# Kernel tuning notes

Hardware: AMD Instinct MI355X
Metric: run time of the kernel (lower is better)

Reference implementation:

```python
import jax, jax.numpy as jnp
import numpy as np

NEG = -1e9  # matches deepblast's -1e10-style boundary fill, fp32-safe


def nw_terminal(theta, A):
    # Soft Needleman-Wunsch forward pass with the softmax (logsumexp) operator,
    # vectorized as an anti-diagonal wavefront scan.
    # theta, A: [N, M]. Returns terminal value V[N, M].
    # Recursion (deepblast): V[i,j] = theta[i-1,j-1] +
    #   lse(A[i-1,j-1] + V[i-1,j], V[i-1,j-1], A[i-1,j-1] + V[i,j-1])
    N, M = theta.shape
    ii = jnp.arange(N + 1)  # row index along a diagonal
    prev2 = jnp.full((N + 1,), NEG, theta.dtype).at[0].set(0.0)  # diagonal k=0: V[0,0]=0
    prev1 = jnp.full((N + 1,), NEG, theta.dtype)                  # diagonal k=1: boundary
    neg1 = jnp.full((1,), NEG, theta.dtype)

    def step(carry, k):
        p2, p1 = carry
        jj = k - ii
        valid = (ii >= 1) & (jj >= 1) & (jj <= M)
        ti = jnp.clip(ii - 1, 0, N - 1)
        tj = jnp.clip(jj - 1, 0, M - 1)
        th = theta[ti, tj]
        a = A[ti, tj]
        up = jnp.concatenate([neg1, p1[:-1]])    # V[i-1, j]
        left = p1                                 # V[i, j-1]
        diag = jnp.concatenate([neg1, p2[:-1]])   # V[i-1, j-1]
        v = jax.nn.logsumexp(jnp.stack([a + up, diag, a + left]), axis=0)
        cur = jnp.where(valid, th + v, NEG)
        return (p1, cur), None

    (_, last), _ = jax.lax.scan(step, (prev2, prev1), jnp.arange(2, N + M + 1))
    return last[N]  # V[N, M]


def nw_decode(theta, A):
    # Expected alignment matrix = d V_terminal / d theta, exactly what
    # NWDecoderCUDA.decode computes via its forward/backward DP passes
    # (gradient taken w.r.t. theta only; A is held fixed).
    f = lambda th: jnp.sum(jax.vmap(nw_terminal)(th, A))
    return jax.grad(f)(theta)


def setup_inputs() -> dict:
    key = jax.random.key(0)
    k1, k2, k3, k4 = jax.random.split(key, 4)
    B, N, M, D = 8, 512, 512, 512
    s = 1.0 / np.sqrt(D)  # keep bilinear scores O(1), as trained embeddings would be
    return {
        "zx": jax.random.normal(k1, (B, N, D), jnp.float32) * s,
        "zy": jax.random.normal(k2, (B, M, D), jnp.float32) * s,
        "gx": jax.random.normal(k3, (B, N, D), jnp.float32) * s,
        "gy": jax.random.normal(k4, (B, M, D), jnp.float32) * s,
    }


def reference(zx, zy, gx, gy):
    theta = jax.nn.softplus(jnp.einsum('bid,bjd->bij', zx, zy))  # match scores [B,N,M]
    A = jax.nn.log_sigmoid(jnp.einsum('bid,bjd->bij', gx, gy))   # gap scores   [B,N,M]
    aln = nw_decode(theta, A)                                     # soft alignment [B,N,M]
    return aln, theta, A
```

## Files before the change

kernel.cpp:

```cpp
#include <hip/hip_runtime.h>
#include <cmath>

#define NEG -1e9f
#define LOG2E 1.44269504088896340736f
constexpr int B = 8, N = 512, M = 512, D = 512;
constexpr size_t NM = (size_t)N * M;

constexpr int NCHUNK = 72;

#define EXP2F(x) __builtin_amdgcn_exp2f(x)
#define LOG2F(x) __builtin_amdgcn_logf(x)

typedef float f32x2 __attribute__((ext_vector_type(2)));

#define GLOAD(dst, ptr) \
    asm volatile("global_load_dwordx2 %0, %1, off" : "=v"(dst) : "v"(ptr))

__device__ __forceinline__ float dpp_shr1(float v) {
    return __int_as_float(__builtin_amdgcn_update_dpp(
        __float_as_int(v), __float_as_int(v), 0x138, 0xf, 0xf, false));
}
__device__ __forceinline__ float dpp_shl1(float v) {
    return __int_as_float(__builtin_amdgcn_update_dpp(
        __float_as_int(v), __float_as_int(v), 0x130, 0xf, 0xf, false));
}

__device__ __forceinline__ int diag_off(int kd) {
    return (kd <= 511) ? ((kd * (kd + 1)) >> 1)
                       : ((int)NM - (((1023 - kd) * (1024 - kd)) >> 1));
}

__global__ __launch_bounds__(256)
void gemm_act_kernel(const float* __restrict__ zx, const float* __restrict__ zy,
                     const float* __restrict__ gx, const float* __restrict__ gy,
                     float* __restrict__ out_theta, float* __restrict__ out_A)
{
    const int bz = blockIdx.z;
    const int b = bz >> 1, which = bz & 1;
    const float* X = (which ? gx : zx) + (size_t)b * N * D;
    const float* Y = (which ? gy : zy) + (size_t)b * M * D;
    float* C = (which ? out_A : out_theta) + (size_t)b * NM;

    __shared__ float Xs[16][68];
    __shared__ float Ys[16][68];

    const int tx = threadIdx.x, ty = threadIdx.y;
    const int t = ty * 16 + tx;
    const int lrow = t >> 2;
    const int lk4 = (t & 3) * 4;
    const int row0 = blockIdx.y * 64, col0 = blockIdx.x * 64;

    float acc[4][4] = {};

    for (int k0 = 0; k0 < D; k0 += 16) {
        const float4 xv = *(const float4*)&X[(row0 + lrow) * D + k0 + lk4];
        const float4 yv = *(const float4*)&Y[(col0 + lrow) * D + k0 + lk4];
        Xs[lk4 + 0][lrow] = xv.x; Xs[lk4 + 1][lrow] = xv.y;
        Xs[lk4 + 2][lrow] = xv.z; Xs[lk4 + 3][lrow] = xv.w;
        Ys[lk4 + 0][lrow] = yv.x; Ys[lk4 + 1][lrow] = yv.y;
        Ys[lk4 + 2][lrow] = yv.z; Ys[lk4 + 3][lrow] = yv.w;
        __syncthreads();
#pragma unroll
        for (int kk = 0; kk < 16; kk++) {
            const float4 a = *(const float4*)&Xs[kk][ty * 4];
            const float4 bb = *(const float4*)&Ys[kk][tx * 4];
            acc[0][0] += a.x * bb.x; acc[0][1] += a.x * bb.y; acc[0][2] += a.x * bb.z; acc[0][3] += a.x * bb.w;
            acc[1][0] += a.y * bb.x; acc[1][1] += a.y * bb.y; acc[1][2] += a.y * bb.z; acc[1][3] += a.y * bb.w;
            acc[2][0] += a.z * bb.x; acc[2][1] += a.z * bb.y; acc[2][2] += a.z * bb.z; acc[2][3] += a.z * bb.w;
            acc[3][0] += a.w * bb.x; acc[3][1] += a.w * bb.y; acc[3][2] += a.w * bb.z; acc[3][3] += a.w * bb.w;
        }
        __syncthreads();
    }

#pragma unroll
    for (int r = 0; r < 4; r++) {
        float4 o;
        float* op = &o.x;
#pragma unroll
        for (int c = 0; c < 4; c++) {
            const float x = acc[r][c];
            const float l = log1pf(expf(-fabsf(x)));
            op[c] = which ? (fminf(x, 0.0f) - l)
                          : (fmaxf(x, 0.0f) + l);
        }
        *(float4*)&C[(size_t)(row0 + ty * 4 + r) * M + col0 + tx * 4] = o;
    }
}

__global__ __launch_bounds__(256)
void reorder_in_kernel(const float* __restrict__ theta, const float* __restrict__ A,
                       float2* __restrict__ TAD)
{
    __shared__ float T[64][67];
    __shared__ float Ag[64][67];
    const int b = blockIdx.z;
    const float* ts = theta + (size_t)b * NM;
    const float* as = A + (size_t)b * NM;
    float2* dst = TAD + (size_t)b * NM;
    const int r0 = blockIdx.y * 64, c0 = blockIdx.x * 64;
    const int t = threadIdx.x, lane = t & 63, wv = t >> 6;

#pragma unroll
    for (int e = 0; e < 16; e++) {
        const int r = wv * 16 + e;
        T[r][lane]  = ts[(size_t)(r0 + r) * M + c0 + lane];
        Ag[r][lane] = as[(size_t)(r0 + r) * M + c0 + lane];
    }
    __syncthreads();
    for (int dd = wv; dd < 127; dd += 4) {
        const int kd = r0 + c0 + dd;
        const int rlo = max(0, dd - 63);
        const int L = min(63, dd) - rlo + 1;
        if (lane < L) {
            const int rloc = rlo + lane;
            const int gr = r0 + rloc;
            dst[diag_off(kd) + gr - max(0, kd - 511)] =
                make_float2(T[rloc][dd - rloc] * LOG2E, Ag[rloc][dd - rloc] * LOG2E);
        }
    }
}

__global__ __launch_bounds__(256)
void reorder_out_kernel(const float* __restrict__ ED, float* __restrict__ aln)
{
    __shared__ float T[64][67];
    const int b = blockIdx.z;
    const float* src = ED + (size_t)b * NM;
    float* dst = aln + (size_t)b * NM;
    const int r0 = blockIdx.y * 64, c0 = blockIdx.x * 64;
    const int t = threadIdx.x, lane = t & 63, wv = t >> 6;

    for (int dd = wv; dd < 127; dd += 4) {
        const int kd = r0 + c0 + dd;
        const int rlo = max(0, dd - 63);
        const int L = min(63, dd) - rlo + 1;
        if (lane < L) {
            const int rloc = rlo + lane;
            const int gr = r0 + rloc;
            T[rloc][dd - rloc] = src[diag_off(kd) + gr - max(0, kd - 511)];
        }
    }
    __syncthreads();
#pragma unroll
    for (int e = 0; e < 16; e++) {
        const int r = wv * 16 + e;
        dst[(size_t)(r0 + r) * M + c0 + lane] = T[r][lane];
    }
}

#define VMCNT_TOP_PF                                        \
    if (pf) { asm volatile("s_waitcnt vmcnt(16)"); }        \
    else    { asm volatile("s_waitcnt vmcnt(0)");  }        \
    __builtin_amdgcn_sched_barrier(0);

#define CHUNK_BARRIER                          \
    __builtin_amdgcn_sched_barrier(0);         \
    asm volatile("s_waitcnt lgkmcnt(0)");      \
    __builtin_amdgcn_s_barrier();              \
    __builtin_amdgcn_sched_barrier(0);

#define DECL16(P)  f32x2 P##0, P##1, P##2, P##3, P##4, P##5, P##6, P##7, \
                         P##8, P##9, P##10, P##11, P##12, P##13, P##14, P##15;
#define DECL16F(P) float P##0, P##1, P##2, P##3, P##4, P##5, P##6, P##7, \
                         P##8, P##9, P##10, P##11, P##12, P##13, P##14, P##15;

#define FLOAD1(dst) {                                          \
    asm volatile("global_load_dwordx2 %0, %1, %2"              \
                 : "=v"(dst) : "v"(off8l), "s"(tab));          \
    const int d_ = (kdl <= 510) ? max(kdl + 1, 0)              \
                                : max(1022 - kdl, 0);          \
    off8l += d_ * 8; kdl++;                                    \
}
#define F_ISSUE(P) {                                           \
    FLOAD1(P##0)  FLOAD1(P##1)  FLOAD1(P##2)  FLOAD1(P##3)     \
    FLOAD1(P##4)  FLOAD1(P##5)  FLOAD1(P##6)  FLOAD1(P##7)     \
    FLOAD1(P##8)  FLOAD1(P##9)  FLOAD1(P##10) FLOAD1(P##11)    \
    FLOAD1(P##12) FLOAD1(P##13) FLOAD1(P##14) FLOAD1(P##15)    \
}

#define F_CORE(kd_, TA, sh1v, dgv, O) {                        \
    const float th = (TA).x, a = (TA).y;                       \
    const float x0 = a + sh1v;                                 \
    const float x2 = a + vprev;                                \
    const float mx = fmaxf(fmaxf(x0, dgv), x2);                \
    const float e0 = EXP2F(x0 - mx);                           \
    const float e1 = EXP2F(dgv - mx);                          \
    const float e2 = EXP2F(x2 - mx);                           \
    const float sum = e0 + e1 + e2;                            \
    const float inv = __builtin_amdgcn_rcpf(sum);              \
    (O).x = e0 * inv; (O).y = e2 * inv;                        \
    vprev = th + mx + LOG2F(sum);                              \
}

#define F_STEP_I(s, TA, O, RG) {                               \
    float sh1 = dpp_shr1(vprev);                               \
    if (lane == 0) sh1 = RG;                                   \
    const float dgv = sh1_d;                                   \
    sh1_d = sh1;                                               \
    F_CORE(kb + (s), TA, sh1, dgv, O)                          \
    wv##s = vprev;                                             \
}

#define F_STEP_G(s, TA, O, RG) {                               \
    const int kd = kb + (s);                                   \
    const int jj = kd - tid;                                   \
    float sh1 = dpp_shr1(vprev);                               \
    if (lane == 0) sh1 = RG;                                   \
    const float dgv = (jj == 0) ? ((tid == 0) ? 0.0f : NEG) : sh1_d; \
    sh1_d = sh1;                                               \
    if (jj >= 0 && jj < M) { F_CORE(kd, TA, sh1, dgv, O) }     \
    wv##s = vprev;                                             \
}

#define F_STEPS(SFX, CUR)                                                      \
    F_STEP_##SFX(0,  CUR##0,  o0,  rgP) F_STEP_##SFX(1,  CUR##1,  o1,  g0)     \
    F_STEP_##SFX(2,  CUR##2,  o2,  g1)  F_STEP_##SFX(3,  CUR##3,  o3,  g2)     \
    F_STEP_##SFX(4,  CUR##4,  o4,  g3)  F_STEP_##SFX(5,  CUR##5,  o5,  g4)     \
    F_STEP_##SFX(6,  CUR##6,  o6,  g5)  F_STEP_##SFX(7,  CUR##7,  o7,  g6)     \
    F_STEP_##SFX(8,  CUR##8,  o8,  g7)  F_STEP_##SFX(9,  CUR##9,  o9,  g8)     \
    F_STEP_##SFX(10, CUR##10, o10, g9)  F_STEP_##SFX(11, CUR##11, o11, g10)    \
    F_STEP_##SFX(12, CUR##12, o12, g11) F_STEP_##SFX(13, CUR##13, o13, g12)    \
    F_STEP_##SFX(14, CUR##14, o14, g13) F_STEP_##SFX(15, CUR##15, o15, g14)

#define F_ADV_S { const int d_ = (kds <= 510) ? (kds + 1) : (1022 - kds);    \
                  off8s += d_ * 8; kds++; }
#define FST_I(O) {                                                           \
    asm volatile("global_store_dwordx2 %0, %1, %2"                           \
                 :: "v"(off8s), "v"(O), "s"(pb) : "memory");                 \
    F_ADV_S }
#define FST_G(s, O) {                                                        \
    const int jj = kb + (s) - tid;                                           \
    if (jj >= 0 && jj < M) {                                                 \
        asm volatile("global_store_dwordx2 %0, %1, %2"                       \
                     :: "v"(off8s), "v"(O), "s"(pb) : "memory"); }           \
    F_ADV_S }
#define F_STORES_I {                                                         \
    FST_I(o0)  FST_I(o1)  FST_I(o2)  FST_I(o3)                               \
    FST_I(o4)  FST_I(o5)  FST_I(o6)  FST_I(o7)                               \
    FST_I(o8)  FST_I(o9)  FST_I(o10) FST_I(o11)                              \
    FST_I(o12) FST_I(o13) FST_I(o14) FST_I(o15) }
#define F_STORES_G {                                                         \
    FST_G(0,o0)   FST_G(1,o1)   FST_G(2,o2)   FST_G(3,o3)                    \
    FST_G(4,o4)   FST_G(5,o5)   FST_G(6,o6)   FST_G(7,o7)                    \
    FST_G(8,o8)   FST_G(9,o9)   FST_G(10,o10) FST_G(11,o11)                  \
    FST_G(12,o12) FST_G(13,o13) FST_G(14,o14) FST_G(15,o15) }

#define F_CHUNK(c_, CUR, NXT) {                                \
    const int c = (c_);                                        \
    VMCNT_TOP_PF                      \
    F_ISSUE(NXT)               \
    const int kb = 16 * c - w16;                               \
    const int kr = kb - 64 * w;                                \
    const bool act = (c >= ca && c <= cb);                     \
    const bool interior = act && (kr >= 64) && (kr <= 496);    \
    const float rgP = gcar;                                    \
    if (w > 0 && c >= ca - 1 && c <= cb) {                     \
        const float4* rp = (const float4*)&ring[w - 1][kb & 63]; \
        const float4 A0 = rp[0], A1 = rp[1];                   \
        const float4 A2 = rp[2], A3 = rp[3];                   \
        g0  = A0.x; g1  = A0.y; g2  = A0.z; g3  = A0.w;        \
        g4  = A1.x; g5  = A1.y; g6  = A1.z; g7  = A1.w;        \
        g8  = A2.x; g9  = A2.y; g10 = A2.z; g11 = A2.w;        \
        g12 = A3.x; g13 = A3.y; g14 = A3.z; g15 = A3.w;        \
        gcar = g15;                                            \
    }                                                          \
    if (act) {                                                 \
        DECL16F(wv)                                            \
        DECL16(o)                                              \
        if (interior) {                                        \
            F_STEPS(I, CUR)                                    \
            F_STORES_I                                         \
        } else {                                               \
            F_STEPS(G, CUR)                                    \
            F_STORES_G                                         \
        }                                                      \
        if (lane == 63) {                                      \
            float4* wp = (float4*)&ring[w][kb & 63];           \
            wp[0] = make_float4(wv0,  wv1,  wv2,  wv3);        \
            wp[1] = make_float4(wv4,  wv5,  wv6,  wv7);        \
            wp[2] = make_float4(wv8,  wv9,  wv10, wv11);       \
            wp[3] = make_float4(wv12, wv13, wv14, wv15);       \
        }                                                      \
    }                                                          \
    pf = interior;                                             \
    CHUNK_BARRIER                                              \
}

__global__ __launch_bounds__(512, 1)
void nw_forward_kernel(const float2* __restrict__ TAD, float2* __restrict__ pD)
{
    __shared__ __align__(16) float ring[8][64];
    const int b = blockIdx.x;
    const int tid = threadIdx.x;
    const int w = __builtin_amdgcn_readfirstlane(tid >> 6);
    const int lane = tid & 63;
    const int w16 = 16 * w;
    const float2* tab = TAD + (size_t)b * NM;
    float2* pb = pD + (size_t)b * NM;

    for (int x = tid; x < 8 * 64; x += 512) ((float*)ring)[x] = NEG;
    __syncthreads();

    const int ca = 5 * w, cb = 5 * w + 35;

    int kdl = -w16;
    int off8l = tid * 8;
    int kds = 64 * w;
    int off8s = (((kds * (kds + 1)) >> 1) + tid) * 8;

    DECL16(fa) DECL16(fb)
    F_ISSUE(fa)

    float g0 = NEG, g1 = NEG, g2 = NEG, g3 = NEG, g4 = NEG, g5 = NEG,
          g6 = NEG, g7 = NEG, g8 = NEG, g9 = NEG, g10 = NEG, g11 = NEG,
          g12 = NEG, g13 = NEG, g14 = NEG, g15 = NEG, gcar = NEG;

    float vprev = NEG, sh1_d = NEG;
    bool pf = false;

#pragma unroll 1
    for (int c2 = 0; c2 < NCHUNK; c2 += 2) {
        F_CHUNK(c2 + 0, fa, fb)
        F_CHUNK(c2 + 1, fb, fa)
    }
}

#define BLOAD1(dst) {                                          \
    asm volatile("global_load_dwordx2 %0, %1, %2"              \
                 : "=v"(dst) : "v"(off8l), "s"(pbp));          \
    const int d_ = (kdl <= 511) ? (-max(kdl, 0))               \
                                : min(kdl - 1023, 0);          \
    off8l += d_ * 8; kdl--;                                    \
}
#define B_ISSUE(P) {                                           \
    BLOAD1(P##0)  BLOAD1(P##1)  BLOAD1(P##2)  BLOAD1(P##3)     \
    BLOAD1(P##4)  BLOAD1(P##5)  BLOAD1(P##6)  BLOAD1(P##7)     \
    BLOAD1(P##8)  BLOAD1(P##9)  BLOAD1(P##10) BLOAD1(P##11)    \
    BLOAD1(P##12) BLOAD1(P##13) BLOAD1(P##14) BLOAD1(P##15)    \
}

#define B_CORE(kd_, PP, suv, sdv, EV, TERMFIX) {               \
    float e = suv + sdv + ql1;                                 \
    TERMFIX                                                    \
    const float pu = (PP).x, pl = (PP).y;                      \
    const float pd = 1.0f - pu - pl;                           \
    const float qu = pu * e, qd = pd * e, ql = pl * e;         \
    EV = e;                                                    \
    qd2 = qd1; qd1 = qd; qu1 = qu; ql1 = ql;                   \
}

#define B_STEP_I(s, PP, EV, RU, RD) {                          \
    float su = dpp_shl1(qu1);                                  \
    float sd = dpp_shl1(qd2);                                  \
    if (lane == 63) { su = RU; sd = RD; }                      \
    B_CORE(kb - (s), PP, su, sd, EV, )                         \
    wu##s = qu1; wd##s = qd1;                                  \
}

#define B_STEP_G(s, PP, EV, RU, RD) {                          \
    const int kd = kb - (s);                                   \
    const int jj = kd - tid;                                   \
    float su = dpp_shl1(qu1);                                  \
    float sd = dpp_shl1(qd2);                                  \
    if (lane == 63) { su = RU; sd = RD; }                      \
    if (jj >= 0 && jj < M) {                                   \
        B_CORE(kd, PP, su, sd, EV,                             \
               if (tid == N - 1 && jj == M - 1) e = 1.0f;)     \
    }                                                          \
    wu##s = qu1; wd##s = qd1;                                  \
}

#define B_STEPS(SFX, CUR)                                        \
    B_STEP_##SFX(0,  CUR##0,  ev0,  cuP,  cAP)                   \
    B_STEP_##SFX(1,  CUR##1,  ev1,  gu15, cBP)                   \
    B_STEP_##SFX(2,  CUR##2,  ev2,  gu14, gd15)                  \
    B_STEP_##SFX(3,  CUR##3,  ev3,  gu13, gd14)                  \
    B_STEP_##SFX(4,  CUR##4,  ev4,  gu12, gd13)                  \
    B_STEP_##SFX(5,  CUR##5,  ev5,  gu11, gd12)                  \
    B_STEP_##SFX(6,  CUR##6,  ev6,  gu10, gd11)                  \
    B_STEP_##SFX(7,  CUR##7,  ev7,  gu9,  gd10)                  \
    B_STEP_##SFX(8,  CUR##8,  ev8,  gu8,  gd9)                   \
    B_STEP_##SFX(9,  CUR##9,  ev9,  gu7,  gd8)                   \
    B_STEP_##SFX(10, CUR##10, ev10, gu6,  gd7)                   \
    B_STEP_##SFX(11, CUR##11, ev11, gu5,  gd6)                   \
    B_STEP_##SFX(12, CUR##12, ev12, gu4,  gd5)                   \
    B_STEP_##SFX(13, CUR##13, ev13, gu3,  gd4)                   \
    B_STEP_##SFX(14, CUR##14, ev14, gu2,  gd3)                   \
    B_STEP_##SFX(15, CUR##15, ev15, gu1,  gd2)

#define B_ADV_S { const int d_ = (kds <= 511) ? (-max(kds, 0))               \
                                              : min(kds - 1023, 0);          \
                  off4s += d_ * 4; kds--; }
#define BST_I(EV) {                                                          \
    asm volatile("global_store_dword %0, %1, %2"                             \
                 :: "v"(off4s), "v"(EV), "s"(ebp) : "memory");               \
    B_ADV_S }
#define BST_G(s, EV) {                                                       \
    const int jj = kb - (s) - tid;                                           \
    if (jj >= 0 && jj < M) {                                                 \
        asm volatile("global_store_dword %0, %1, %2"                         \
                     :: "v"(off4s), "v"(EV), "s"(ebp) : "memory"); }         \
    B_ADV_S }
#define B_STORES_I {                                                         \
    BST_I(ev0)  BST_I(ev1)  BST_I(ev2)  BST_I(ev3)                           \
    BST_I(ev4)  BST_I(ev5)  BST_I(ev6)  BST_I(ev7)                           \
    BST_I(ev8)  BST_I(ev9)  BST_I(ev10) BST_I(ev11)                          \
    BST_I(ev12) BST_I(ev13) BST_I(ev14) BST_I(ev15) }
#define B_STORES_G {                                                         \
    BST_G(0,ev0)   BST_G(1,ev1)   BST_G(2,ev2)   BST_G(3,ev3)                \
    BST_G(4,ev4)   BST_G(5,ev5)   BST_G(6,ev6)   BST_G(7,ev7)                \
    BST_G(8,ev8)   BST_G(9,ev9)   BST_G(10,ev10) BST_G(11,ev11)              \
    BST_G(12,ev12) BST_G(13,ev13) BST_G(14,ev14) BST_G(15,ev15) }

#define B_CHUNK(c_, CUR, NXT) {                                \
    const int c = (c_);                                        \
    VMCNT_TOP_PF                                               \
    B_ISSUE(NXT)                                               \
    const int kb = 1134 - 16 * c - w16;                        \
    const int krb = kb - 64 * w;                               \
    const bool act = (c >= ca && c <= cb);                     \
    const bool interior = act && (krb >= 78) && (krb <= 511);  \
    const float cuP = cu, cAP = cA, cBP = cB;                  \
    if (w < 7 && c >= ca - 1 && c <= cb) {                     \
        const int rb = (kb - 14) & 63;                         \
        const float4* up = (const float4*)&ring_u[w + 1][rb];  \
        const float4 U0 = up[0], U1 = up[1];                   \
        const float4 U2 = up[2], U3 = up[3];                   \
        gu0  = U0.x; gu1  = U0.y; gu2  = U0.z; gu3  = U0.w;    \
        gu4  = U1.x; gu5  = U1.y; gu6  = U1.z; gu7  = U1.w;    \
        gu8  = U2.x; gu9  = U2.y; gu10 = U2.z; gu11 = U2.w;    \
        gu12 = U3.x; gu13 = U3.y; gu14 = U3.z; gu15 = U3.w;    \
        const float4* dp = (const float4*)&ring_d[w + 1][rb];  \
        const float4 D0 = dp[0], D1 = dp[1];                   \
        const float4 D2 = dp[2], D3 = dp[3];                   \
        gd0  = D0.x; gd1  = D0.y; gd2  = D0.z; gd3  = D0.w;    \
        gd4  = D1.x; gd5  = D1.y; gd6  = D1.z; gd7  = D1.w;    \
        gd8  = D2.x; gd9  = D2.y; gd10 = D2.z; gd11 = D2.w;    \
        gd12 = D3.x; gd13 = D3.y; gd14 = D3.z; gd15 = D3.w;    \
        cu = gu0; cA = gd1; cB = gd0;                          \
    }                                                          \
    if (act) {                                                 \
        DECL16F(wu) DECL16F(wd) DECL16F(ev)                    \
        if (interior) {                                        \
            B_STEPS(I, CUR)                                    \
            B_STORES_I                                         \
        } else {                                               \
            B_STEPS(G, CUR)                                    \
            B_STORES_G                                         \
        }                                                      \
        if (lane == 0) {                                       \
            const int rb2 = (kb - 14) & 63;                    \
            float4* au = (float4*)&ring_u[w][rb2];             \
            au[0] = make_float4(wu15, wu14, wu13, wu12);       \
            au[1] = make_float4(wu11, wu10, wu9,  wu8);        \
            au[2] = make_float4(wu7,  wu6,  wu5,  wu4);        \
            au[3] = make_float4(wu3,  wu2,  wu1,  wu0);        \
            float4* ad = (float4*)&ring_d[w][rb2];             \
            ad[0] = make_float4(wd15, wd14, wd13, wd12);       \
            ad[1] = make_float4(wd11, wd10, wd9,  wd8);        \
            ad[2] = make_float4(wd7,  wd6,  wd5,  wd4);        \
            ad[3] = make_float4(wd3,  wd2,  wd1,  wd0);        \
        }                                                      \
    }                                                          \
    pf = interior;                                             \
    CHUNK_BARRIER                                              \
}

__global__ __launch_bounds__(512, 1)
void nw_backward_kernel(const float2* __restrict__ pD, float* __restrict__ ED)
{
    __shared__ __align__(16) float ring_u[8][64];
    __shared__ __align__(16) float ring_d[8][64];
    const int b = blockIdx.x;
    const int tid = threadIdx.x;
    const int w = __builtin_amdgcn_readfirstlane(tid >> 6);
    const int lane = tid & 63;
    const int w16 = 16 * w;
    const float2* pbp = pD + (size_t)b * NM;
    float* ebp = ED + (size_t)b * NM;

    for (int x = tid; x < 8 * 64; x += 512) {
        ((float*)ring_u)[x] = 0.0f;
        ((float*)ring_d)[x] = 0.0f;
    }
    __syncthreads();

    const int ca = 35 - 5 * w, cb = 70 - 5 * w;

    int kdl = 1134 - w16;
    int off8l = ((int)NM - 512 + tid) * 8;
    int kds = 574 + 64 * w;
    const int am_ = 1023 - kds, bm_ = 1024 - kds;
    int off4s = ((int)NM - ((am_ * bm_) >> 1) + tid - (kds - 511)) * 4;

    DECL16(ba) DECL16(bb)
    B_ISSUE(ba)

    float gu0 = 0.f, gu1 = 0.f, gu2 = 0.f, gu3 = 0.f, gu4 = 0.f, gu5 = 0.f,
          gu6 = 0.f, gu7 = 0.f, gu8 = 0.f, gu9 = 0.f, gu10 = 0.f, gu11 = 0.f,
          gu12 = 0.f, gu13 = 0.f, gu14 = 0.f, gu15 = 0.f;
    float gd0 = 0.f, gd1 = 0.f, gd2 = 0.f, gd3 = 0.f, gd4 = 0.f, gd5 = 0.f,
          gd6 = 0.f, gd7 = 0.f, gd8 = 0.f, gd9 = 0.f, gd10 = 0.f, gd11 = 0.f,
          gd12 = 0.f, gd13 = 0.f, gd14 = 0.f, gd15 = 0.f;
    float cu = 0.f, cA = 0.f, cB = 0.f;

    float qu1 = 0.0f, qd1 = 0.0f, qd2 = 0.0f, ql1 = 0.0f;
    bool pf = false;

#pragma unroll 1
    for (int c2 = 0; c2 < NCHUNK; c2 += 2) {
        B_CHUNK(c2 + 0, ba, bb)
        B_CHUNK(c2 + 1, bb, ba)
    }
}

extern "C" void kernel_launch(void* const* d_in, const int* in_sizes, int n_in,
                              void* d_out, int out_size, void* d_ws, size_t ws_size,
                              hipStream_t stream) {
    const float* zx = (const float*)d_in[0];
    const float* zy = (const float*)d_in[1];
    const float* gx = (const float*)d_in[2];
    const float* gy = (const float*)d_in[3];

    float* aln   = (float*)d_out;
    float* theta = aln + B * NM;
    float* Amat  = theta + B * NM;

    float2* TAD = (float2*)d_ws;
    float2* pD  = TAD + B * NM;
    float*  ED  = (float*)d_ws;

    gemm_act_kernel<<<dim3(8, 8, B * 2), dim3(16, 16), 0, stream>>>(zx, zy, gx, gy, theta, Amat);
    reorder_in_kernel<<<dim3(8, 8, B), 256, 0, stream>>>(theta, Amat, TAD);
    nw_forward_kernel<<<B, 512, 0, stream>>>(TAD, pD);
    nw_backward_kernel<<<B, 512, 0, stream>>>(pD, ED);
    reorder_out_kernel<<<dim3(8, 8, B), 256, 0, stream>>>(ED, aln);
}
```

Before: 502.8 us.

## Halve wavefront barriers by widening warp skew to two chunks; deepen GEMM K tile

The forward and backward wavefront kernels now issue a workgroup barrier only every second chunk. To keep this safe, the skew between consecutive warps grows from one chunk to two (32 diagonals), and the chunk count and active ranges are extended to match. Separately, the GEMM prologue kernel loads a K-slab of 32 instead of 16 per shared-memory stage, halving its barrier count. The trade-off is a longer pipeline fill and drain (78 chunks instead of 72) in exchange for fewer synchronisations, and correctness depends on the 64-entry ring buffer tolerating the wider lag.

```diff
diff --git a/kernel.cpp b/kernel.cpp
--- a/kernel.cpp
+++ b/kernel.cpp
@@ -6,15 +6,12 @@
 constexpr int B = 8, N = 512, M = 512, D = 512;
 constexpr size_t NM = (size_t)N * M;
 
-constexpr int NCHUNK = 72;
+constexpr int NCHUNK = 78;
 
 #define EXP2F(x) __builtin_amdgcn_exp2f(x)
 #define LOG2F(x) __builtin_amdgcn_logf(x)
 
 typedef float f32x2 __attribute__((ext_vector_type(2)));
-
-#define GLOAD(dst, ptr) \
-    asm volatile("global_load_dwordx2 %0, %1, off" : "=v"(dst) : "v"(ptr))
 
 __device__ __forceinline__ float dpp_shr1(float v) {
     return __int_as_float(__builtin_amdgcn_update_dpp(
@@ -41,8 +38,8 @@
     const float* Y = (which ? gy : zy) + (size_t)b * M * D;
     float* C = (which ? out_A : out_theta) + (size_t)b * NM;
 
-    __shared__ float Xs[16][68];
-    __shared__ float Ys[16][68];
+    __shared__ float Xs[32][68];
+    __shared__ float Ys[32][68];
 
     const int tx = threadIdx.x, ty = threadIdx.y;
     const int t = ty * 16 + tx;
@@ -52,16 +49,22 @@
 
     float acc[4][4] = {};
 
-    for (int k0 = 0; k0 < D; k0 += 16) {
-        const float4 xv = *(const float4*)&X[(row0 + lrow) * D + k0 + lk4];
-        const float4 yv = *(const float4*)&Y[(col0 + lrow) * D + k0 + lk4];
-        Xs[lk4 + 0][lrow] = xv.x; Xs[lk4 + 1][lrow] = xv.y;
-        Xs[lk4 + 2][lrow] = xv.z; Xs[lk4 + 3][lrow] = xv.w;
-        Ys[lk4 + 0][lrow] = yv.x; Ys[lk4 + 1][lrow] = yv.y;
-        Ys[lk4 + 2][lrow] = yv.z; Ys[lk4 + 3][lrow] = yv.w;
+    for (int k0 = 0; k0 < D; k0 += 32) {
+        const float4 xv0 = *(const float4*)&X[(row0 + lrow) * D + k0 + lk4];
+        const float4 xv1 = *(const float4*)&X[(row0 + lrow) * D + k0 + 16 + lk4];
+        const float4 yv0 = *(const float4*)&Y[(col0 + lrow) * D + k0 + lk4];
+        const float4 yv1 = *(const float4*)&Y[(col0 + lrow) * D + k0 + 16 + lk4];
+        Xs[lk4 + 0][lrow] = xv0.x; Xs[lk4 + 1][lrow] = xv0.y;
+        Xs[lk4 + 2][lrow] = xv0.z; Xs[lk4 + 3][lrow] = xv0.w;
+        Xs[lk4 + 16][lrow] = xv1.x; Xs[lk4 + 17][lrow] = xv1.y;
+        Xs[lk4 + 18][lrow] = xv1.z; Xs[lk4 + 19][lrow] = xv1.w;
+        Ys[lk4 + 0][lrow] = yv0.x; Ys[lk4 + 1][lrow] = yv0.y;
+        Ys[lk4 + 2][lrow] = yv0.z; Ys[lk4 + 3][lrow] = yv0.w;
+        Ys[lk4 + 16][lrow] = yv1.x; Ys[lk4 + 17][lrow] = yv1.y;
+        Ys[lk4 + 18][lrow] = yv1.z; Ys[lk4 + 19][lrow] = yv1.w;
         __syncthreads();
 #pragma unroll
-        for (int kk = 0; kk < 16; kk++) {
+        for (int kk = 0; kk < 32; kk++) {
             const float4 a = *(const float4*)&Xs[kk][ty * 4];
             const float4 bb = *(const float4*)&Ys[kk][tx * 4];
             acc[0][0] += a.x * bb.x; acc[0][1] += a.x * bb.y; acc[0][2] += a.x * bb.z; acc[0][3] += a.x * bb.w;
@@ -245,11 +248,11 @@
     FST_G(8,o8)   FST_G(9,o9)   FST_G(10,o10) FST_G(11,o11)                  \
     FST_G(12,o12) FST_G(13,o13) FST_G(14,o14) FST_G(15,o15) }
 
-#define F_CHUNK(c_, CUR, NXT) {                                \
+#define F_CHUNK(c_, CUR, NXT, BAR) {                           \
     const int c = (c_);                                        \
     VMCNT_TOP_PF                      \
     F_ISSUE(NXT)               \
-    const int kb = 16 * c - w16;                               \
+    const int kb = 16 * c - w32;                               \
     const int kr = kb - 64 * w;                                \
     const bool act = (c >= ca && c <= cb);                     \
     const bool interior = act && (kr >= 64) && (kr <= 496);    \
@@ -283,7 +286,7 @@
         }                                                      \
     }                                                          \
     pf = interior;                                             \
-    CHUNK_BARRIER                                              \
+    BAR                                                        \
 }
 
 __global__ __launch_bounds__(512, 1)
@@ -294,16 +297,16 @@
     const int tid = threadIdx.x;
     const int w = __builtin_amdgcn_readfirstlane(tid >> 6);
     const int lane = tid & 63;
-    const int w16 = 16 * w;
+    const int w32 = 32 * w;
     const float2* tab = TAD + (size_t)b * NM;
     float2* pb = pD + (size_t)b * NM;
 
     for (int x = tid; x < 8 * 64; x += 512) ((float*)ring)[x] = NEG;
     __syncthreads();
 
-    const int ca = 5 * w, cb = 5 * w + 35;
-
-    int kdl = -w16;
+    const int ca = 6 * w, cb = 6 * w + 35;
+
+    int kdl = -w32;
     int off8l = tid * 8;
     int kds = 64 * w;
     int off8s = (((kds * (kds + 1)) >> 1) + tid) * 8;
@@ -320,8 +323,8 @@
 
 #pragma unroll 1
     for (int c2 = 0; c2 < NCHUNK; c2 += 2) {
-        F_CHUNK(c2 + 0, fa, fb)
-        F_CHUNK(c2 + 1, fb, fa)
+        F_CHUNK(c2 + 0, fa, fb, )
+        F_CHUNK(c2 + 1, fb, fa, CHUNK_BARRIER)
     }
 }
 
@@ -412,11 +415,11 @@
     BST_G(8,ev8)   BST_G(9,ev9)   BST_G(10,ev10) BST_G(11,ev11)              \
     BST_G(12,ev12) BST_G(13,ev13) BST_G(14,ev14) BST_G(15,ev15) }
 
-#define B_CHUNK(c_, CUR, NXT) {                                \
+#define B_CHUNK(c_, CUR, NXT, BAR) {                           \
     const int c = (c_);                                        \
     VMCNT_TOP_PF                                               \
     B_ISSUE(NXT)                                               \
-    const int kb = 1134 - 16 * c - w16;                        \
+    const int kb = 1246 - 16 * c - w32;                        \
     const int krb = kb - 64 * w;                               \
     const bool act = (c >= ca && c <= cb);                     \
     const bool interior = act && (krb >= 78) && (krb <= 511);  \
@@ -463,7 +466,7 @@
         }                                                      \
     }                                                          \
     pf = interior;                                             \
-    CHUNK_BARRIER                                              \
+    BAR                                                        \
 }
 
 __global__ __launch_bounds__(512, 1)
@@ -475,7 +478,7 @@
     const int tid = threadIdx.x;
     const int w = __builtin_amdgcn_readfirstlane(tid >> 6);
     const int lane = tid & 63;
-    const int w16 = 16 * w;
+    const int w32 = 32 * w;
     const float2* pbp = pD + (size_t)b * NM;
     float* ebp = ED + (size_t)b * NM;
 
@@ -485,9 +488,9 @@
     }
     __syncthreads();
 
-    const int ca = 35 - 5 * w, cb = 70 - 5 * w;
-
-    int kdl = 1134 - w16;
+    const int ca = 42 - 6 * w, cb = 77 - 6 * w;
+
+    int kdl = 1246 - w32;
     int off8l = ((int)NM - 512 + tid) * 8;
     int kds = 574 + 64 * w;
     const int am_ = 1023 - kds, bm_ = 1024 - kds;
@@ -509,8 +512,8 @@
 
 #pragma unroll 1
     for (int c2 = 0; c2 < NCHUNK; c2 += 2) {
-        B_CHUNK(c2 + 0, ba, bb)
-        B_CHUNK(c2 + 1, bb, ba)
+        B_CHUNK(c2 + 0, ba, bb, )
+        B_CHUNK(c2 + 1, bb, ba, CHUNK_BARRIER)
     }
 }
 
```

New measurement: 510.2 us. No clear change (+1.5%).
